# Kernel optimization log

Measured on AMD Instinct MI355X. Metric: run time of the kernel, lower is better.

The kernel has to match this reference:

```python
import jax, jax.numpy as jnp
import numpy as np
from jax import lax

BN_EPS = 1e-5


def setup_inputs() -> dict:
    key = jax.random.key(0)
    k1, k2, k3, k4, k5, k6 = jax.random.split(key, 6)
    N, Cin, H, W = 32, 512, 56, 56
    Cout = 32
    Ctot = 1024
    return {
        "x_slice": jax.random.normal(k1, (N, Cin, H, W), dtype=jnp.float32),
        "out_map": jnp.zeros((N, Ctot, H, W), dtype=jnp.float32),
        "bn_weight": jax.random.uniform(k2, (Cin,), dtype=jnp.float32, minval=0.5, maxval=1.5),
        "bn_bias": jax.random.normal(k3, (Cin,), dtype=jnp.float32) * 0.1,
        "running_mean": jax.random.normal(k4, (Cin,), dtype=jnp.float32) * 0.1,
        "running_var": jax.random.uniform(k5, (Cin,), dtype=jnp.float32, minval=0.5, maxval=1.5),
        "conv_weight": jax.random.normal(k6, (Cout, Cin, 3, 3), dtype=jnp.float32) * 0.02,
        "write_offset": 512,
    }


def reference(x_slice, out_map, bn_weight, bn_bias, running_mean, running_var, conv_weight, write_offset):
    # BatchNorm with running stats (inference normalization), fused scale/shift
    inv_std = lax.rsqrt(running_var + BN_EPS)            # [C]
    scale = (bn_weight * inv_std)[None, :, None, None]   # [1,C,1,1]
    shift = (bn_bias - running_mean * bn_weight * inv_std)[None, :, None, None]
    relu_out = jnp.maximum(x_slice * scale + shift, 0.0)  # BN + ReLU fused
    # 3x3 conv, padding=1, no bias (NCHW / OIHW)
    conv_out = lax.conv_general_dilated(
        relu_out, conv_weight,
        window_strides=(1, 1), padding=((1, 1), (1, 1)),
        dimension_numbers=("NCHW", "OIHW", "NCHW"))
    # write into offset slice of the preallocated feature map, return the slice
    out_map = lax.dynamic_update_slice_in_dim(out_map, conv_out, write_offset, axis=1)
    Cout = conv_weight.shape[0]
    return lax.dynamic_slice_in_dim(out_map, write_offset, Cout, axis=1)
```

## Files before the change

### kernel.cpp

```cpp
#include <hip/hip_runtime.h>
#include <cstdint>

#define CIN    512
#define COUT   32
#define IMH    56
#define IMW    56
#define NB     32
#define CHUNKS 16
#define XSTR   40
#define NTH    512
#define YT     7
#define SLOTS  2240
#define SPT    5
#define BUFS   (10 * 58 * XSTR)

typedef __attribute__((ext_vector_type(8))) short v8s;
typedef __attribute__((ext_vector_type(4))) float v4f;

__device__ __forceinline__ unsigned short f2bf(float f) {
    unsigned u = __builtin_bit_cast(unsigned, f);
    u += 0x7FFFu + ((u >> 16) & 1u);
    return (unsigned short)(u >> 16);
}

__global__ void wtransform(const float* __restrict__ cw,
                           const float* __restrict__ bn_w, const float* __restrict__ bn_b,
                           const float* __restrict__ rm,   const float* __restrict__ rv,
                           unsigned short* __restrict__ w2, float4* __restrict__ bq) {
    int idx = blockIdx.x * blockDim.x + threadIdx.x;
    if (idx < 256) {
        int c = idx * 2;
        float s0 = bn_w[c]     * rsqrtf(rv[c]     + 1e-5f);
        float s1 = bn_w[c + 1] * rsqrtf(rv[c + 1] + 1e-5f);
        bq[idx] = make_float4(s0, bn_b[c] - rm[c] * s0, s1, bn_b[c + 1] - rm[c + 1] * s1);
    }
    if (idx >= CHUNKS * 9 * 2 * 64 * 8) return;
    int j    = idx & 7;
    int lane = (idx >> 3) & 63;
    int mt   = (idx >> 9) & 1;
    int tmp  = idx >> 10;
    int tap  = tmp % 9;
    int gc   = tmp / 9;
    int m = mt * 16 + (lane & 15);
    int k = gc * 32 + (lane >> 4) * 8 + j;
    w2[idx] = f2bf(cw[((size_t)m * CIN + k) * 9 + tap]);
}

struct SlotTab {
    int lbase[SPT];
    int gofs[SPT];
    int actm;
};

__device__ __forceinline__ void load_inputs(const float* __restrict__ p0,
                                            const SlotTab& st,
                                            float4 (&va)[SPT], float4 (&vb)[SPT]) {
    #pragma unroll
    for (int j = 0; j < SPT; ++j) {
        if (st.actm & (1 << j)) {
            const float* p = p0 + st.gofs[j];
            va[j] = *(const float4*)p;
            vb[j] = *(const float4*)(p + 3136);
        }
    }
}

__device__ __forceinline__ unsigned cvtpk(float lo, float hi) {
    unsigned r;
    asm("v_cvt_pk_bf16_f32 %0, %1, %2" : "=v"(r) : "v"(lo), "v"(hi));
    return r;
}

__device__ __forceinline__ void pack_chunk(unsigned short* __restrict__ bp,
                                           const SlotTab& st, float4 bn,
                                           const float4 (&va)[SPT], const float4 (&vb)[SPT]) {
    #pragma unroll
    for (int j = 0; j < SPT; ++j) {
        if (st.actm & (1 << j)) {
            float a0 = fmaxf(fmaf(va[j].x, bn.x, bn.y), 0.f);
            float a1 = fmaxf(fmaf(va[j].y, bn.x, bn.y), 0.f);
            float a2 = fmaxf(fmaf(va[j].z, bn.x, bn.y), 0.f);
            float a3 = fmaxf(fmaf(va[j].w, bn.x, bn.y), 0.f);
            float b0 = fmaxf(fmaf(vb[j].x, bn.z, bn.w), 0.f);
            float b1 = fmaxf(fmaf(vb[j].y, bn.z, bn.w), 0.f);
            float b2 = fmaxf(fmaf(vb[j].z, bn.z, bn.w), 0.f);
            float b3 = fmaxf(fmaf(vb[j].w, bn.z, bn.w), 0.f);
            unsigned u0 = cvtpk(a0, b0);
            unsigned u1 = cvtpk(a1, b1);
            unsigned u2 = cvtpk(a2, b2);
            unsigned u3 = cvtpk(a3, b3);
            int base = st.lbase[j];
            *(unsigned*)&bp[base]            = u0;
            *(unsigned*)&bp[base + XSTR]     = u1;
            *(unsigned*)&bp[base + 2 * XSTR] = u2;
            *(unsigned*)&bp[base + 3 * XSTR] = u3;
        }
    }
}

__device__ __forceinline__ void mfma_chunk(const unsigned short* __restrict__ bp,
                                           const v8s (&aw0)[9], const v8s (&aw1)[9],
                                           int pbase, bool active,
                                           v4f (&acc)[4][2]) {
    if (!active) return;
    v8s sav0, sav1, sav2;
    #pragma unroll
    for (int i = 0; i < 4; ++i) {
        #pragma unroll
        for (int ty = 0; ty < 3; ++ty) {
            #pragma unroll
            for (int tx = 0; tx < 3; ++tx) {
                v8s b;
                if (ty == 0 && i > 0) {
                    b = (tx == 0) ? sav0 : (tx == 1) ? sav1 : sav2;
                } else {
                    b = *(const v8s*)&bp[pbase + ((2 * i + ty) * 58 + tx) * XSTR];
                }
                if (ty == 2) {
                    if (tx == 0) sav0 = b; else if (tx == 1) sav1 = b; else sav2 = b;
                }
                const int tap = ty * 3 + tx;
                acc[i][0] = __builtin_amdgcn_mfma_f32_16x16x32_bf16(aw0[tap], b, acc[i][0], 0, 0, 0);
                acc[i][1] = __builtin_amdgcn_mfma_f32_16x16x32_bf16(aw1[tap], b, acc[i][1], 0, 0, 0);
            }
        }
    }
}

__device__ __forceinline__ void do_chunk(int gc, const float* __restrict__ xn,
                                         const unsigned short* __restrict__ w2,
                                         const float4* __restrict__ s_bq,
                                         unsigned short* __restrict__ bp,
                                         const SlotTab& st,
                                         float4 (&va)[SPT], float4 (&vb)[SPT],
                                         int pbase, bool active,
                                         v4f (&acc)[4][2], int c2, int lane,
                                         bool prefetch) {
    v8s aw0[9], aw1[9];
    const v8s* wpv = (const v8s*)(w2 + (size_t)gc * 9216);
    #pragma unroll
    for (int t = 0; t < 9; ++t) {
        aw0[t] = wpv[t * 128 + lane];
        aw1[t] = wpv[t * 128 + 64 + lane];
    }

    float4 bn = s_bq[gc * 16 + c2];

    pack_chunk(bp, st, bn, va, vb);

    if (prefetch)
        load_inputs(xn + (size_t)(gc + 2) * 32 * 3136, st, va, vb);

    asm volatile("s_waitcnt lgkmcnt(0)" ::: "memory");
    __builtin_amdgcn_s_barrier();

    mfma_chunk(bp, aw0, aw1, pbase, active, acc);
}

__global__ __launch_bounds__(NTH, 1)
void conv_mfma(const float* __restrict__ x,
               const unsigned short* __restrict__ w2,
               const float4* __restrict__ bq,
               float* __restrict__ out)
{
    __shared__ __align__(16) unsigned short s_x[2][BUFS];
    __shared__ __align__(16) float4 s_bq[CHUNKS * 16];

    const int tid  = threadIdx.x;
    const int lane = tid & 63;
    const int wv   = tid >> 6;

    const int bid = blockIdx.x;
    const int k8  = bid & 7;
    const int q   = bid >> 3;
    const int n   = k8 + 8 * (q / 7);
    const int yt  = q % 7;
    const int y0   = yt * 8;
    const int c2   = tid & 15;

    if (tid < CHUNKS * 16) s_bq[tid] = bq[tid];

    SlotTab st;
    st.actm = 0;
    #pragma unroll
    for (int j = 0; j < SPT; ++j) {
        int slot = tid + j * NTH;
        bool inr = (slot < SLOTS);
        int rest = slot >> 4;
        int xg = rest % 14;
        int r  = rest / 14;
        int iy = y0 - 1 + r;
        bool v = inr && (iy >= 0) && (iy < IMH);
        if (v) st.actm |= (1 << j);
        st.lbase[j] = (r * 58 + xg * 4 + 1) * XSTR + c2 * 2;
        st.gofs[j]  = c2 * 2 * 3136 + (v ? iy : 0) * 56 + xg * 4;
    }

    for (int i = tid; i < 2 * 10 * 2 * 20; i += NTH) {
        int kq = i % 20;
        int t  = i / 20;
        int side = t & 1;
        int r  = (t >> 1) % 10;
        int b  = t / 20;
        *(unsigned*)&s_x[b][(r * 58 + (side ? 57 : 0)) * XSTR + kq * 2] = 0u;
    }
    if (yt == 0 || yt == YT - 1) {
        int r = (yt == 0) ? 0 : 9;
        for (int i = tid; i < 2 * 58 * 20; i += NTH) {
            int b = i >= 58 * 20;
            int q2 = i - b * 58 * 20;
            *(unsigned*)&s_x[b][r * 58 * XSTR + q2 * 2] = 0u;
        }
    }

    const bool active = (wv < 7);
    const int dy  = (lane & 15) >> 3;
    const int px8 = lane & 7;
    const int pbase = (dy * 58 + wv * 8 + px8) * XSTR + (lane >> 4) * 8;
    v4f acc[4][2];
    const v4f zero4 = {0.f, 0.f, 0.f, 0.f};
    #pragma unroll
    for (int i = 0; i < 4; ++i) { acc[i][0] = zero4; acc[i][1] = zero4; }

    const float* xn = x + (size_t)n * CIN * 3136;

    float4 vaA[SPT], vbA[SPT], vaB[SPT], vbB[SPT];
    load_inputs(xn, st, vaA, vbA);
    load_inputs(xn + (size_t)32 * 3136, st, vaB, vbB);

    asm volatile("s_waitcnt lgkmcnt(0)" ::: "memory");
    __builtin_amdgcn_s_barrier();

    for (int gc = 0; gc < CHUNKS; gc += 2) {
        do_chunk(gc,     xn, w2, s_bq, &s_x[0][0], st, vaA, vbA,
                 pbase, active, acc, c2, lane, gc + 2 < CHUNKS);
        do_chunk(gc + 1, xn, w2, s_bq, &s_x[1][0], st, vaB, vbB,
                 pbase, active, acc, c2, lane, gc + 3 < CHUNKS);
    }

    if (active) {
        const int prow = (lane >> 4) * 4;
        #pragma unroll
        for (int i = 0; i < 4; ++i) {
            int py = 2 * i + dy;
            int px = wv * 8 + px8;
            size_t o0 = (size_t)n * COUT * 3136 + (size_t)(y0 + py) * 56 + px;
            #pragma unroll
            for (int mt = 0; mt < 2; ++mt) {
                #pragma unroll
                for (int r = 0; r < 4; ++r) {
                    int cout = mt * 16 + prow + r;
                    out[o0 + (size_t)cout * 3136] = acc[i][mt][r];
                }
            }
        }
    }
}

extern "C" void kernel_launch(void* const* d_in, const int* in_sizes, int n_in,
                              void* d_out, int out_size, void* d_ws, size_t ws_size,
                              hipStream_t stream) {
    const float* x      = (const float*)d_in[0];
    const float* bn_w   = (const float*)d_in[2];
    const float* bn_b   = (const float*)d_in[3];
    const float* r_mean = (const float*)d_in[4];
    const float* r_var  = (const float*)d_in[5];
    const float* cw     = (const float*)d_in[6];
    float* out = (float*)d_out;

    unsigned short* w2 = (unsigned short*)d_ws;
    float4* bq = (float4*)((char*)d_ws + 294912);

    wtransform<<<dim3(576), dim3(256), 0, stream>>>(cw, bn_w, bn_b, r_mean, r_var, w2, bq);

    conv_mfma<<<dim3(YT * NB), dim3(NTH), 0, stream>>>(x, w2, bq, out);
}
```

Baseline: 71.49 us.

## Software-pipeline LDS packing of next chunk with MFMA on current chunk

Restructures the chunk loop so each step packs the next input chunk into the alternate LDS buffer while running MFMAs on the already-packed current buffer, with a single barrier afterward. A prologue packs chunk 0 up front, and the global prefetch distance shifts by one chunk. This is meant to overlap BN+ReLU packing and LDS writes with matrix compute instead of serializing them around a barrier. It may raise register pressure and adds a prologue step.

```diff
diff --git a/kernel.cpp b/kernel.cpp
--- a/kernel.cpp
+++ b/kernel.cpp
@@ -130,12 +130,13 @@
 __device__ __forceinline__ void do_chunk(int gc, const float* __restrict__ xn,
                                          const unsigned short* __restrict__ w2,
                                          const float4* __restrict__ s_bq,
-                                         unsigned short* __restrict__ bp,
+                                         const unsigned short* __restrict__ bp_read,
+                                         unsigned short* __restrict__ bp_write,
                                          const SlotTab& st,
                                          float4 (&va)[SPT], float4 (&vb)[SPT],
                                          int pbase, bool active,
                                          v4f (&acc)[4][2], int c2, int lane,
-                                         bool prefetch) {
+                                         bool do_pack, bool do_pref) {
     v8s aw0[9], aw1[9];
     const v8s* wpv = (const v8s*)(w2 + (size_t)gc * 9216);
     #pragma unroll
@@ -144,17 +145,18 @@
         aw1[t] = wpv[t * 128 + 64 + lane];
     }
 
-    float4 bn = s_bq[gc * 16 + c2];
-
-    pack_chunk(bp, st, bn, va, vb);
-
-    if (prefetch)
-        load_inputs(xn + (size_t)(gc + 2) * 32 * 3136, st, va, vb);
+    if (do_pack) {
+        float4 bn = s_bq[(gc + 1) * 16 + c2];
+        pack_chunk(bp_write, st, bn, va, vb);
+    }
+
+    if (do_pref)
+        load_inputs(xn + (size_t)(gc + 3) * 32 * 3136, st, va, vb);
+
+    mfma_chunk(bp_read, aw0, aw1, pbase, active, acc);
 
     asm volatile("s_waitcnt lgkmcnt(0)" ::: "memory");
     __builtin_amdgcn_s_barrier();
-
-    mfma_chunk(bp, aw0, aw1, pbase, active, acc);
 }
 
 __global__ __launch_bounds__(NTH, 1)
@@ -231,11 +233,19 @@
     asm volatile("s_waitcnt lgkmcnt(0)" ::: "memory");
     __builtin_amdgcn_s_barrier();
 
+    {
+        float4 bn0 = s_bq[c2];
+        pack_chunk(&s_x[0][0], st, bn0, vaA, vbA);
+        load_inputs(xn + (size_t)2 * 32 * 3136, st, vaA, vbA);
+    }
+    asm volatile("s_waitcnt lgkmcnt(0)" ::: "memory");
+    __builtin_amdgcn_s_barrier();
+
     for (int gc = 0; gc < CHUNKS; gc += 2) {
-        do_chunk(gc,     xn, w2, s_bq, &s_x[0][0], st, vaA, vbA,
-                 pbase, active, acc, c2, lane, gc + 2 < CHUNKS);
-        do_chunk(gc + 1, xn, w2, s_bq, &s_x[1][0], st, vaB, vbB,
-                 pbase, active, acc, c2, lane, gc + 3 < CHUNKS);
+        do_chunk(gc,     xn, w2, s_bq, &s_x[0][0], &s_x[1][0], st, vaB, vbB,
+                 pbase, active, acc, c2, lane, gc + 1 < CHUNKS, gc + 3 < CHUNKS);
+        do_chunk(gc + 1, xn, w2, s_bq, &s_x[1][0], &s_x[0][0], st, vaA, vbA,
+                 pbase, active, acc, c2, lane, gc + 2 < CHUNKS, gc + 4 < CHUNKS);
     }
 
     if (active) {
```

Result: slower. 76.63 us (+7.2%).

## Rebalance MFMA work so the idle eighth wave computes spare tiles

Applied to the files above, without the earlier changes.

Previously only 7 of 8 waves ran MFMAs, each handling 4 row-pair tiles of an 8-pixel column. Now waves 4-6 hand off their last tile to wave 7, which computes three tiles from different columns without reusing halo rows. Every wave then does 3 or 4 tiles, which shortens the critical path of the MFMA phase per chunk. The cost is some extra LDS reads in wave 7, which cannot reuse loaded rows, and more per-wave branching.

```diff
diff --git a/kernel.cpp b/kernel.cpp
--- a/kernel.cpp
+++ b/kernel.cpp
@@ -98,30 +98,50 @@
     }
 }
 
-__device__ __forceinline__ void mfma_chunk(const unsigned short* __restrict__ bp,
+__device__ __forceinline__ void mfma_chain(const unsigned short* __restrict__ bp,
                                            const v8s (&aw0)[9], const v8s (&aw1)[9],
-                                           int pbase, bool active,
+                                           const int (&tb)[4], int ntile,
                                            v4f (&acc)[4][2]) {
-    if (!active) return;
     v8s sav0, sav1, sav2;
     #pragma unroll
-    for (int i = 0; i < 4; ++i) {
+    for (int t = 0; t < 4; ++t) {
+        if (t < ntile) {
+            #pragma unroll
+            for (int ty = 0; ty < 3; ++ty) {
+                #pragma unroll
+                for (int tx = 0; tx < 3; ++tx) {
+                    v8s b;
+                    if (ty == 0 && t > 0) {
+                        b = (tx == 0) ? sav0 : (tx == 1) ? sav1 : sav2;
+                    } else {
+                        b = *(const v8s*)&bp[tb[t] + (ty * 58 + tx) * XSTR];
+                    }
+                    if (ty == 2) {
+                        if (tx == 0) sav0 = b; else if (tx == 1) sav1 = b; else sav2 = b;
+                    }
+                    const int tap = ty * 3 + tx;
+                    acc[t][0] = __builtin_amdgcn_mfma_f32_16x16x32_bf16(aw0[tap], b, acc[t][0], 0, 0, 0);
+                    acc[t][1] = __builtin_amdgcn_mfma_f32_16x16x32_bf16(aw1[tap], b, acc[t][1], 0, 0, 0);
+                }
+            }
+        }
+    }
+}
+
+__device__ __forceinline__ void mfma_fresh(const unsigned short* __restrict__ bp,
+                                           const v8s (&aw0)[9], const v8s (&aw1)[9],
+                                           const int (&tb)[4],
+                                           v4f (&acc)[4][2]) {
+    #pragma unroll
+    for (int t = 0; t < 3; ++t) {
         #pragma unroll
         for (int ty = 0; ty < 3; ++ty) {
             #pragma unroll
             for (int tx = 0; tx < 3; ++tx) {
-                v8s b;
-                if (ty == 0 && i > 0) {
-                    b = (tx == 0) ? sav0 : (tx == 1) ? sav1 : sav2;
-                } else {
-                    b = *(const v8s*)&bp[pbase + ((2 * i + ty) * 58 + tx) * XSTR];
-                }
-                if (ty == 2) {
-                    if (tx == 0) sav0 = b; else if (tx == 1) sav1 = b; else sav2 = b;
-                }
+                v8s b = *(const v8s*)&bp[tb[t] + (ty * 58 + tx) * XSTR];
                 const int tap = ty * 3 + tx;
-                acc[i][0] = __builtin_amdgcn_mfma_f32_16x16x32_bf16(aw0[tap], b, acc[i][0], 0, 0, 0);
-                acc[i][1] = __builtin_amdgcn_mfma_f32_16x16x32_bf16(aw1[tap], b, acc[i][1], 0, 0, 0);
+                acc[t][0] = __builtin_amdgcn_mfma_f32_16x16x32_bf16(aw0[tap], b, acc[t][0], 0, 0, 0);
+                acc[t][1] = __builtin_amdgcn_mfma_f32_16x16x32_bf16(aw1[tap], b, acc[t][1], 0, 0, 0);
             }
         }
     }
@@ -133,7 +153,7 @@
                                          unsigned short* __restrict__ bp,
                                          const SlotTab& st,
                                          float4 (&va)[SPT], float4 (&vb)[SPT],
-                                         int pbase, bool active,
+                                         const int (&tb)[4], int wv, int ntile,
                                          v4f (&acc)[4][2], int c2, int lane,
                                          bool prefetch) {
     v8s aw0[9], aw1[9];
@@ -154,7 +174,8 @@
     asm volatile("s_waitcnt lgkmcnt(0)" ::: "memory");
     __builtin_amdgcn_s_barrier();
 
-    mfma_chunk(bp, aw0, aw1, pbase, active, acc);
+    if (wv < 7) mfma_chain(bp, aw0, aw1, tb, ntile, acc);
+    else        mfma_fresh(bp, aw0, aw1, tb, acc);
 }
 
 __global__ __launch_bounds__(NTH, 1)
@@ -213,10 +234,17 @@
         }
     }
 
-    const bool active = (wv < 7);
+    const int ntile = (wv < 4) ? 4 : 3;
     const int dy  = (lane & 15) >> 3;
     const int px8 = lane & 7;
-    const int pbase = (dy * 58 + wv * 8 + px8) * XSTR + (lane >> 4) * 8;
+    int tb[4];
+    #pragma unroll
+    for (int t = 0; t < 4; ++t) {
+        int col, ii;
+        if (wv < 7) { col = wv;                 ii = (t < ntile) ? t : 0; }
+        else        { col = 4 + ((t < 3) ? t : 0); ii = 3; }
+        tb[t] = ((2 * ii + dy) * 58 + col * 8 + px8) * XSTR + (lane >> 4) * 8;
+    }
     v4f acc[4][2];
     const v4f zero4 = {0.f, 0.f, 0.f, 0.f};
     #pragma unroll
@@ -233,25 +261,25 @@
 
     for (int gc = 0; gc < CHUNKS; gc += 2) {
         do_chunk(gc,     xn, w2, s_bq, &s_x[0][0], st, vaA, vbA,
-                 pbase, active, acc, c2, lane, gc + 2 < CHUNKS);
+                 tb, wv, ntile, acc, c2, lane, gc + 2 < CHUNKS);
         do_chunk(gc + 1, xn, w2, s_bq, &s_x[1][0], st, vaB, vbB,
-                 pbase, active, acc, c2, lane, gc + 3 < CHUNKS);
-    }
-
-    if (active) {
-        const int prow = (lane >> 4) * 4;
+                 tb, wv, ntile, acc, c2, lane, gc + 3 < CHUNKS);
+    }
+
+    const int prow = (lane >> 4) * 4;
+    #pragma unroll
+    for (int t = 0; t < 4; ++t) {
+        if (t >= ntile) break;
+        int py, px;
+        if (wv < 7) { py = 2 * t + dy; px = wv * 8 + px8; }
+        else        { py = 6 + dy;     px = (4 + t) * 8 + px8; }
+        size_t o0 = (size_t)n * COUT * 3136 + (size_t)(y0 + py) * 56 + px;
         #pragma unroll
-        for (int i = 0; i < 4; ++i) {
-            int py = 2 * i + dy;
-            int px = wv * 8 + px8;
-            size_t o0 = (size_t)n * COUT * 3136 + (size_t)(y0 + py) * 56 + px;
+        for (int mt = 0; mt < 2; ++mt) {
             #pragma unroll
-            for (int mt = 0; mt < 2; ++mt) {
-                #pragma unroll
-                for (int r = 0; r < 4; ++r) {
-                    int cout = mt * 16 + prow + r;
-                    out[o0 + (size_t)cout * 3136] = acc[i][mt][r];
-                }
+            for (int r = 0; r < 4; ++r) {
+                int cout = mt * 16 + prow + r;
+                out[o0 + (size_t)cout * 3136] = acc[t][mt][r];
             }
         }
     }
```

Measured after the change: 86.86 us. 21.5% more time.
